# Kernel tuning notes

Hardware: AMD Instinct MI355X
Metric: run time of the kernel (lower is better)

Reference implementation:

```python
import jax, jax.numpy as jnp
import numpy as np

KERNEL = 3
STRIDE = 1
DILATION = 1
EPS = 1e-8


def setup_inputs() -> dict:
    key = jax.random.key(0)
    ks = jax.random.split(key, 7)
    b, dim, dim_out, dim_embed, n = 8, 512, 512, 512, 4
    h = w = 64
    fmap = jax.random.normal(ks[0], (b, dim, h, w), dtype=jnp.float32)
    embed = jax.random.normal(ks[1], (b, dim_embed), dtype=jnp.float32)
    # base conv kernel bank [n, o, i, k, k] (kaiming-normal-ish init)
    fan_in = dim * KERNEL * KERNEL
    weights = jax.random.normal(ks[2], (n, dim_out, dim, KERNEL, KERNEL), dtype=jnp.float32) * np.sqrt(2.0 / fan_in)
    # to_mod: Linear(dim_embed, dim)
    mod_w = jax.random.normal(ks[3], (dim, dim_embed), dtype=jnp.float32) / np.sqrt(dim_embed)
    mod_b = jnp.zeros((dim,), dtype=jnp.float32)
    # to_adaptive_weight: Linear(dim_embed, n)
    adapt_w = jax.random.normal(ks[4], (n, dim_embed), dtype=jnp.float32) / np.sqrt(dim_embed)
    adapt_b = jnp.zeros((n,), dtype=jnp.float32)
    return {"fmap": fmap, "embed": embed, "weights": weights,
            "mod_w": mod_w, "mod_b": mod_b, "adapt_w": adapt_w, "adapt_b": adapt_b}


def reference(fmap, embed, weights, mod_w, mod_b, adapt_w, adapt_b):
    b, _, h, w_sp = fmap.shape
    # adaptive kernel selection: softmax over n kernels, per sample
    sel = jax.nn.softmax(embed @ adapt_w.T + adapt_b, axis=-1)          # [b, n]
    wts = jnp.einsum('noikl,bn->boikl', weights, sel)                   # [b, o, i, k, k]
    # modulation
    mod = embed @ mod_w.T + mod_b                                       # [b, i]
    wts = wts * (mod[:, None, :, None, None] + 1.0)
    # demodulation: normalize each (b, o) filter
    inv_norm = jax.lax.rsqrt(jnp.clip(jnp.sum(wts * wts, axis=(2, 3, 4), keepdims=True), EPS))
    wts = wts * inv_norm
    # grouped conv with groups = b
    pad = ((h - 1) * (STRIDE - 1) + DILATION * (KERNEL - 1)) // 2
    x = fmap.reshape(1, b * fmap.shape[1], h, w_sp)                     # [1, b*i, h, w]
    wg = wts.reshape(b * wts.shape[1], wts.shape[2], KERNEL, KERNEL)    # [b*o, i, k, k]
    out = jax.lax.conv_general_dilated(
        x, wg,
        window_strides=(STRIDE, STRIDE),
        padding=[(pad, pad), (pad, pad)],
        rhs_dilation=(DILATION, DILATION),
        dimension_numbers=('NCHW', 'OIHW', 'NCHW'),
        feature_group_count=b,
    )                                                                   # [1, b*o, h', w']
    return out.reshape(b, -1, out.shape[2], out.shape[3])
```

## Files before the change

kernel.cpp:

```cpp
#include <hip/hip_runtime.h>
#include <stdint.h>

typedef short s16x8 __attribute__((ext_vector_type(8)));
typedef __bf16 bf16x8 __attribute__((ext_vector_type(8)));
typedef float f32x4 __attribute__((ext_vector_type(4)));

#define NB 8
#define DIM 512
#define DIMO 512
#define DEMB 512
#define NKER 4
#define HH 64
#define WW 64
#define HP 66
#define WP 72
#define KTOT 4608
#define NIT 36

__device__ __forceinline__ unsigned short f2bf(float f) {
  unsigned int u = __builtin_bit_cast(unsigned int, f);
  u += 0x7fffu + ((u >> 16) & 1u);
  return (unsigned short)(u >> 16);
}

__global__ void prep_all(const float* __restrict__ fmap,
                         const float* __restrict__ embed,
                         const float* __restrict__ mod_w,
                         const float* __restrict__ mod_b,
                         const float* __restrict__ adapt_w,
                         const float* __restrict__ adapt_b,
                         unsigned short* __restrict__ xt,
                         float* __restrict__ mod, float* __restrict__ sel) {
  const int bid = blockIdx.x;
  const int t = threadIdx.x;

  if (bid < 528) {
    const int b = bid / 66;
    const int yp = bid - b * 66;
    unsigned short* rowb = xt + (((size_t)(b * HP + yp)) * WP) * DIM;
    uint4 z; z.x = 0; z.y = 0; z.z = 0; z.w = 0;

    if (yp == 0 || yp == HP - 1) {
      uint4* p = (uint4*)rowb;
#pragma unroll
      for (int r = 0; r < 18; ++r) p[t + r * 256] = z;
      return;
    }
#pragma unroll
    for (int r = 0; r < 2; ++r) {
      int idx = t + r * 256;
      int pxi = idx >> 6;
      int px = pxi ? (64 + pxi) : 0;
      ((uint4*)(rowb + (size_t)px * DIM))[idx & 63] = z;
    }
    const int x = t & 63;
    const int ic0 = (t >> 6) * 8;
    const float* fb = fmap + (size_t)b * DIM * (HH * WW) + (size_t)(yp - 1) * WW + x;
    unsigned short* ob = rowb + (size_t)(x + 1) * DIM;
    for (int r = 0; r < 16; ++r) {
      int i0 = ic0 + r * 32;
      s16x8 vv;
#pragma unroll
      for (int j = 0; j < 8; ++j)
        vv[j] = (short)f2bf(fb[(size_t)(i0 + j) * (HH * WW)]);
      *(s16x8*)&ob[i0] = vv;
    }
    return;
  }

  const int e9 = bid - 528;
  const int b = e9 / 9;
  const int xc = e9 - b * 9;
  const int lane = t & 63, wv = t >> 6;
  const float* e = embed + (size_t)b * DEMB;

  if (xc == 8) {
    if (wv == 0) {
      float lg[NKER];
#pragma unroll
      for (int n = 0; n < NKER; ++n) {
        const float* ar = adapt_w + (size_t)n * DEMB;
        float s = 0.f;
#pragma unroll
        for (int k = 0; k < 8; ++k) s += e[lane + 64 * k] * ar[lane + 64 * k];
#pragma unroll
        for (int off = 32; off; off >>= 1) s += __shfl_xor(s, off);
        lg[n] = s + adapt_b[n];
      }
      if (lane == 0) {
        float m = lg[0];
#pragma unroll
        for (int n = 1; n < NKER; ++n) m = fmaxf(m, lg[n]);
        float ex[NKER], sum = 0.f;
#pragma unroll
        for (int n = 0; n < NKER; ++n) { ex[n] = expf(lg[n] - m); sum += ex[n]; }
#pragma unroll
        for (int n = 0; n < NKER; ++n) sel[b * NKER + n] = ex[n] / sum;
      }
    }
    return;
  }

  float ev[8];
#pragma unroll
  for (int k = 0; k < 8; ++k) ev[k] = e[lane + 64 * k];
  const int i0 = xc * 64 + wv * 16;
  for (int r = 0; r < 16; ++r) {
    const float* wr = mod_w + (size_t)(i0 + r) * DEMB;
    float s = 0.f;
#pragma unroll
    for (int k = 0; k < 8; ++k) s += ev[k] * wr[lane + 64 * k];
#pragma unroll
    for (int off = 32; off; off >>= 1) s += __shfl_xor(s, off);
    if (lane == 0) mod[b * DIM + i0 + r] = s + mod_b[i0 + r];
  }
}

__global__ void prep_weights(const float* __restrict__ wbank,
                             const float* __restrict__ sel,
                             const float* __restrict__ mod,
                             unsigned short* __restrict__ wts) {
  const int o = blockIdx.x;
  const int t = threadIdx.x;
  extern __shared__ float ls[];
  __shared__ float red[8];

#pragma unroll
  for (int n = 0; n < NKER; ++n) {
    const float* wb = wbank + ((size_t)n * DIMO + o) * (DIM * 9);
#pragma unroll
    for (int r = 0; r < 18; ++r) {
      int ii = t + r * 256;
      ls[n * KTOT + ii] = wb[ii];
    }
  }
  __syncthreads();

  const int lane = t & 63, wv = t >> 6;
  for (int b = 0; b < NB; ++b) {
    const float s0 = sel[b * NKER + 0], s1 = sel[b * NKER + 1];
    const float s2 = sel[b * NKER + 2], s3 = sel[b * NKER + 3];
    const float* mo = mod + b * DIM;
    const int par = (b & 1) << 2;

    float v[18];
    float ss = 0.f;
#pragma unroll
    for (int r = 0; r < 18; ++r) {
      int ok = t + r * 256;
      int src = (ok & 511) * 9 + (ok >> 9);
      float w = s0 * ls[src] + s1 * ls[KTOT + src]
              + s2 * ls[2 * KTOT + src] + s3 * ls[3 * KTOT + src];
      w *= (mo[ok & 511] + 1.0f);
      v[r] = w;
      ss += w * w;
    }
    for (int off = 32; off > 0; off >>= 1) ss += __shfl_down(ss, off);
    if (lane == 0) red[wv + par] = ss;
    __syncthreads();
    float tot = red[0 + par] + red[1 + par] + red[2 + par] + red[3 + par];
    float inv = rsqrtf(fmaxf(tot, 1e-8f));
    unsigned short* wo = wts + ((size_t)(b * DIMO + o)) * KTOT;
#pragma unroll
    for (int r = 0; r < 18; ++r)
      wo[t + r * 256] = f2bf(v[r] * inv);
  }
}

__global__ __launch_bounds__(512, 2) void conv_gemm(
    const unsigned short* __restrict__ wts,
    const unsigned short* __restrict__ xt,
    float* __restrict__ out) {
  extern __shared__ __attribute__((aligned(16))) char smem[];

  const int tid = threadIdx.x;
  const int w = tid >> 6, l = tid & 63;
  const int bid0 = blockIdx.x;
  const int bid = ((bid0 & 7) << 5) | (bid0 >> 3);
  const int b = bid >> 5;
  const int mt = (bid >> 4) & 1;
  const int nt = bid & 15;
  const int orow0 = mt << 8;
  const int prow0 = nt << 8;
  const int y0 = nt << 2;
  const int wm = w >> 2, wn = w & 3;
  const int lr = l & 15, lk = l >> 4;

  const unsigned short* a_base = wts + (size_t)(b * 512 + orow0) * KTOT;
  const unsigned short* x_base = xt + (size_t)b * (HP * WP * DIM);

  const int srow = (w << 3) + (l >> 3);
  const int sx8 = (((l & 7) ^ ((l >> 3) & 7)) << 3);
  const int sw0 = ((lk ^ (l & 7)) << 4);
  const int aRow = (((wm << 6) + lr) << 7);
  const int bRow = (((wn << 5) + lr) << 7);

  int pb[2][2];
#pragma unroll
  for (int h = 0; h < 2; ++h)
#pragma unroll
    for (int j = 0; j < 2; ++j) {
      const int pl = (h << 7) + (j << 6) + srow;
      pb[h][j] = (((y0 + (pl >> 6)) * WP + (pl & 63)) << 9);
    }

  f32x4 acc[2][2][4][2] = {};
  s16x8 aF[2][4], bF0[2][2], bF1[2][2];

  auto stageA = [&](int d, int h, int ks) {
#pragma unroll
    for (int j = 0; j < 2; ++j) {
      const unsigned short* gp = a_base + (size_t)((h << 7) + (j << 6) + srow) * KTOT
                               + (ks << 6) + sx8;
      __builtin_amdgcn_global_load_lds(
          (const __attribute__((address_space(1))) void*)gp,
          (__attribute__((address_space(3))) void*)(smem + (d << 16) + (h << 14) + (j << 13) + (w << 10)),
          16, 0, 0);
    }
  };
  auto stageB = [&](int d, int h, int ks) {
    const int t9 = ks >> 3;
    const int ky = (t9 * 11) >> 5;
    const int koff = ky * (WP << 9) + (t9 - 3 * ky) * 512 + ((ks & 7) << 6);
#pragma unroll
    for (int j = 0; j < 2; ++j) {
      const unsigned short* gp = x_base + pb[h][j] + koff + sx8;
      __builtin_amdgcn_global_load_lds(
          (const __attribute__((address_space(1))) void*)gp,
          (__attribute__((address_space(3))) void*)(smem + (d << 16) + 32768 + (h << 14) + (j << 13) + (w << 10)),
          16, 0, 0);
    }
  };

#define VM4 asm volatile("s_waitcnt vmcnt(4)" ::: "memory")
#define VM2 asm volatile("s_waitcnt vmcnt(2)" ::: "memory")
#define VM0 asm volatile("s_waitcnt vmcnt(0)" ::: "memory")
#define FENCE asm volatile("" ::: "memory")
#define BAR do { FENCE; __builtin_amdgcn_s_barrier(); FENCE; } while (0)

#define LOAD_A(d, mq) \
  _Pragma("unroll") for (int s = 0; s < 2; ++s) \
  _Pragma("unroll") for (int mi = 0; mi < 4; ++mi) \
    aF[s][mi] = *(const s16x8*)(smem + ((d) << 16) + ((mq) << 14) + aRow + (mi << 11) + (sw0 ^ (s << 6)));

#define LOAD_B(d, nq, BF) \
  _Pragma("unroll") for (int s = 0; s < 2; ++s) \
  _Pragma("unroll") for (int nj = 0; nj < 2; ++nj) \
    BF[s][nj] = *(const s16x8*)(smem + ((d) << 16) + 32768 + ((nq) << 14) + bRow + (nj << 11) + (sw0 ^ (s << 6)));

#define MFMA_Q(mq, nq, BF) do { \
  __builtin_amdgcn_s_setprio(1); \
  _Pragma("unroll") for (int s = 0; s < 2; ++s) \
  _Pragma("unroll") for (int mi = 0; mi < 4; ++mi) \
  _Pragma("unroll") for (int nj = 0; nj < 2; ++nj) \
    acc[mq][nq][mi][nj] = __builtin_amdgcn_mfma_f32_16x16x32_bf16( \
        __builtin_bit_cast(bf16x8, aF[s][mi]), __builtin_bit_cast(bf16x8, BF[s][nj]), \
        acc[mq][nq][mi][nj], 0, 0, 0); \
  __builtin_amdgcn_s_setprio(0); \
} while (0)

  stageA(0, 0, 0); stageB(0, 0, 0); stageB(0, 1, 0); stageA(0, 1, 0);
  VM4; BAR;

  for (int it = 0; it < NIT - 1; ++it) {
    const int ks1 = 2 * it + 1, ks2 = 2 * it + 2;
    stageA(1, 0, ks1); LOAD_A(0, 0); LOAD_B(0, 0, bF0); VM4; BAR; MFMA_Q(0, 0, bF0);
    stageB(1, 0, ks1); LOAD_B(0, 1, bF1);               VM4; BAR; MFMA_Q(0, 1, bF1);
    stageB(1, 1, ks1); LOAD_A(0, 1);                         BAR; MFMA_Q(1, 1, bF1);
    stageA(1, 1, ks1);                                  VM4; BAR; MFMA_Q(1, 0, bF0);
    stageA(0, 0, ks2); LOAD_A(1, 0); LOAD_B(1, 0, bF0); VM4; BAR; MFMA_Q(0, 0, bF0);
    stageB(0, 0, ks2); LOAD_B(1, 1, bF1);               VM4; BAR; MFMA_Q(0, 1, bF1);
    stageB(0, 1, ks2); LOAD_A(1, 1);                         BAR; MFMA_Q(1, 1, bF1);
    stageA(0, 1, ks2);                                  VM4; BAR; MFMA_Q(1, 0, bF0);
  }
  {
    const int ks1 = 2 * (NIT - 1) + 1;
    stageA(1, 0, ks1); LOAD_A(0, 0); LOAD_B(0, 0, bF0); VM4; BAR; MFMA_Q(0, 0, bF0);
    stageB(1, 0, ks1); LOAD_B(0, 1, bF1);               VM4; BAR; MFMA_Q(0, 1, bF1);
    stageB(1, 1, ks1); LOAD_A(0, 1);                         BAR; MFMA_Q(1, 1, bF1);
    stageA(1, 1, ks1);                                  VM4; BAR; MFMA_Q(1, 0, bF0);
    LOAD_A(1, 0); LOAD_B(1, 0, bF0);                    VM2; BAR; MFMA_Q(0, 0, bF0);
    LOAD_B(1, 1, bF1);                                  VM0; BAR; MFMA_Q(0, 1, bF1);
    LOAD_A(1, 1);                                            BAR; MFMA_Q(1, 1, bF1);
                                                             BAR; MFMA_Q(1, 0, bF0);
  }

#pragma unroll
  for (int mq = 0; mq < 2; ++mq)
#pragma unroll
  for (int nq = 0; nq < 2; ++nq)
#pragma unroll
  for (int mi = 0; mi < 4; ++mi)
#pragma unroll
  for (int nj = 0; nj < 2; ++nj) {
    float* ob = out
      + ((size_t)(b * 512 + orow0 + (mq << 7) + (wm << 6) + (mi << 4) + (lk << 2)) << 12)
      + prow0 + (nq << 7) + (wn << 5) + (nj << 4) + lr;
#pragma unroll
    for (int q = 0; q < 4; ++q)
      ob[(size_t)q << 12] = acc[mq][nq][mi][nj][q];
  }
#undef VM4
#undef VM2
#undef VM0
#undef FENCE
#undef BAR
#undef LOAD_A
#undef LOAD_B
#undef MFMA_Q
}

extern "C" void kernel_launch(void* const* d_in, const int* in_sizes, int n_in,
                              void* d_out, int out_size, void* d_ws, size_t ws_size,
                              hipStream_t stream) {
  const float* fmap    = (const float*)d_in[0];
  const float* embed   = (const float*)d_in[1];
  const float* wbank   = (const float*)d_in[2];
  const float* mod_w   = (const float*)d_in[3];
  const float* mod_b   = (const float*)d_in[4];
  const float* adapt_w = (const float*)d_in[5];
  const float* adapt_b = (const float*)d_in[6];
  float* out = (float*)d_out;

  char* ws = (char*)d_ws;
  float* sel = (float*)ws;
  float* mod = (float*)(ws + 256);
  unsigned short* wts = (unsigned short*)(ws + 256 + 16384);
  unsigned short* xt  = (unsigned short*)(ws + 256 + 16384 + (size_t)NB * DIMO * KTOT * 2);

  prep_all<<<600, 256, 0, stream>>>(fmap, embed, mod_w, mod_b, adapt_w, adapt_b,
                                    xt, mod, sel);

  (void)hipFuncSetAttribute((const void*)prep_weights,
                            hipFuncAttributeMaxDynamicSharedMemorySize, 73728);
  prep_weights<<<512, 256, 73728, stream>>>(wbank, sel, mod, wts);

  (void)hipFuncSetAttribute((const void*)conv_gemm,
                            hipFuncAttributeMaxDynamicSharedMemorySize, 131072);
  conv_gemm<<<dim3(256), dim3(512), 131072, stream>>>(wts, xt, out);
}
```

Before: 163.6 us.

## Split embed prep and co-schedule fmap transpose with weight prep blocks

Moves the small embed projections into their own tiny kernel and merges the fmap pad/transpose work into the weight-prep kernel. Transpose and weight blocks are interleaved across one 1040-block grid so the two bandwidth-bound phases overlap instead of running back to back. The weight prep also caches each thread's 72 bank values in registers and reads mod once per sample, replacing strided shared-memory reads. Risks: higher register pressure, and the transpose blocks launch with 72KB of dynamic shared memory they never use, which can limit occupancy.

```diff
diff --git a/kernel.cpp b/kernel.cpp
--- a/kernel.cpp
+++ b/kernel.cpp
@@ -23,20 +23,74 @@
   return (unsigned short)(u >> 16);
 }
 
-__global__ void prep_all(const float* __restrict__ fmap,
-                         const float* __restrict__ embed,
-                         const float* __restrict__ mod_w,
-                         const float* __restrict__ mod_b,
-                         const float* __restrict__ adapt_w,
-                         const float* __restrict__ adapt_b,
-                         unsigned short* __restrict__ xt,
-                         float* __restrict__ mod, float* __restrict__ sel) {
+__global__ void prep_embed(const float* __restrict__ embed,
+                           const float* __restrict__ mod_w,
+                           const float* __restrict__ mod_b,
+                           const float* __restrict__ adapt_w,
+                           const float* __restrict__ adapt_b,
+                           float* __restrict__ mod, float* __restrict__ sel) {
+  const int bid = blockIdx.x;
+  const int b = bid / 9;
+  const int xc = bid - b * 9;
+  const int t = threadIdx.x;
+  const int lane = t & 63, wv = t >> 6;
+  const float* e = embed + (size_t)b * DEMB;
+
+  if (xc == 8) {
+    if (wv == 0) {
+      float lg[NKER];
+#pragma unroll
+      for (int n = 0; n < NKER; ++n) {
+        const float* ar = adapt_w + (size_t)n * DEMB;
+        float s = 0.f;
+#pragma unroll
+        for (int k = 0; k < 8; ++k) s += e[lane + 64 * k] * ar[lane + 64 * k];
+#pragma unroll
+        for (int off = 32; off; off >>= 1) s += __shfl_xor(s, off);
+        lg[n] = s + adapt_b[n];
+      }
+      if (lane == 0) {
+        float m = lg[0];
+#pragma unroll
+        for (int n = 1; n < NKER; ++n) m = fmaxf(m, lg[n]);
+        float ex[NKER], sum = 0.f;
+#pragma unroll
+        for (int n = 0; n < NKER; ++n) { ex[n] = expf(lg[n] - m); sum += ex[n]; }
+#pragma unroll
+        for (int n = 0; n < NKER; ++n) sel[b * NKER + n] = ex[n] / sum;
+      }
+    }
+    return;
+  }
+
+  float ev[8];
+#pragma unroll
+  for (int k = 0; k < 8; ++k) ev[k] = e[lane + 64 * k];
+  const int i0 = xc * 64 + wv * 16;
+  for (int r = 0; r < 16; ++r) {
+    const float* wr = mod_w + (size_t)(i0 + r) * DEMB;
+    float s = 0.f;
+#pragma unroll
+    for (int k = 0; k < 8; ++k) s += ev[k] * wr[lane + 64 * k];
+#pragma unroll
+    for (int off = 32; off; off >>= 1) s += __shfl_xor(s, off);
+    if (lane == 0) mod[b * DIM + i0 + r] = s + mod_b[i0 + r];
+  }
+}
+
+__global__ void prep_wf(const float* __restrict__ wbank,
+                        const float* __restrict__ sel,
+                        const float* __restrict__ mod,
+                        const float* __restrict__ fmap,
+                        unsigned short* __restrict__ wts,
+                        unsigned short* __restrict__ xt) {
   const int bid = blockIdx.x;
   const int t = threadIdx.x;
 
-  if (bid < 528) {
-    const int b = bid / 66;
-    const int yp = bid - b * 66;
+  if ((bid & 1) && bid < 1024 ? true : bid >= 1024) {
+    const int f = (bid < 1024) ? (bid >> 1) : (bid - 512);
+    const int b = f / 66;
+    const int yp = f - b * 66;
     unsigned short* rowb = xt + (((size_t)(b * HP + yp)) * WP) * DIM;
     uint4 z; z.x = 0; z.y = 0; z.z = 0; z.w = 0;
 
@@ -68,60 +122,7 @@
     return;
   }
 
-  const int e9 = bid - 528;
-  const int b = e9 / 9;
-  const int xc = e9 - b * 9;
-  const int lane = t & 63, wv = t >> 6;
-  const float* e = embed + (size_t)b * DEMB;
-
-  if (xc == 8) {
-    if (wv == 0) {
-      float lg[NKER];
-#pragma unroll
-      for (int n = 0; n < NKER; ++n) {
-        const float* ar = adapt_w + (size_t)n * DEMB;
-        float s = 0.f;
-#pragma unroll
-        for (int k = 0; k < 8; ++k) s += e[lane + 64 * k] * ar[lane + 64 * k];
-#pragma unroll
-        for (int off = 32; off; off >>= 1) s += __shfl_xor(s, off);
-        lg[n] = s + adapt_b[n];
-      }
-      if (lane == 0) {
-        float m = lg[0];
-#pragma unroll
-        for (int n = 1; n < NKER; ++n) m = fmaxf(m, lg[n]);
-        float ex[NKER], sum = 0.f;
-#pragma unroll
-        for (int n = 0; n < NKER; ++n) { ex[n] = expf(lg[n] - m); sum += ex[n]; }
-#pragma unroll
-        for (int n = 0; n < NKER; ++n) sel[b * NKER + n] = ex[n] / sum;
-      }
-    }
-    return;
-  }
-
-  float ev[8];
-#pragma unroll
-  for (int k = 0; k < 8; ++k) ev[k] = e[lane + 64 * k];
-  const int i0 = xc * 64 + wv * 16;
-  for (int r = 0; r < 16; ++r) {
-    const float* wr = mod_w + (size_t)(i0 + r) * DEMB;
-    float s = 0.f;
-#pragma unroll
-    for (int k = 0; k < 8; ++k) s += ev[k] * wr[lane + 64 * k];
-#pragma unroll
-    for (int off = 32; off; off >>= 1) s += __shfl_xor(s, off);
-    if (lane == 0) mod[b * DIM + i0 + r] = s + mod_b[i0 + r];
-  }
-}
-
-__global__ void prep_weights(const float* __restrict__ wbank,
-                             const float* __restrict__ sel,
-                             const float* __restrict__ mod,
-                             unsigned short* __restrict__ wts) {
-  const int o = blockIdx.x;
-  const int t = threadIdx.x;
+  const int o = bid >> 1;
   extern __shared__ float ls[];
   __shared__ float red[8];
 
@@ -135,24 +136,33 @@
     }
   }
   __syncthreads();
+
+  float wreg[NKER][2][9];
+#pragma unroll
+  for (int n = 0; n < NKER; ++n)
+#pragma unroll
+    for (int p = 0; p < 2; ++p)
+#pragma unroll
+      for (int g = 0; g < 9; ++g)
+        wreg[n][p][g] = ls[n * KTOT + (t + p * 256) * 9 + g];
 
   const int lane = t & 63, wv = t >> 6;
   for (int b = 0; b < NB; ++b) {
     const float s0 = sel[b * NKER + 0], s1 = sel[b * NKER + 1];
     const float s2 = sel[b * NKER + 2], s3 = sel[b * NKER + 3];
-    const float* mo = mod + b * DIM;
+    const float m0 = mod[b * DIM + t] + 1.0f;
+    const float m1 = mod[b * DIM + t + 256] + 1.0f;
     const int par = (b & 1) << 2;
 
-    float v[18];
+    float vv[18];
     float ss = 0.f;
 #pragma unroll
     for (int r = 0; r < 18; ++r) {
-      int ok = t + r * 256;
-      int src = (ok & 511) * 9 + (ok >> 9);
-      float w = s0 * ls[src] + s1 * ls[KTOT + src]
-              + s2 * ls[2 * KTOT + src] + s3 * ls[3 * KTOT + src];
-      w *= (mo[ok & 511] + 1.0f);
-      v[r] = w;
+      const int p = r & 1, g = r >> 1;
+      float w = s0 * wreg[0][p][g] + s1 * wreg[1][p][g]
+              + s2 * wreg[2][p][g] + s3 * wreg[3][p][g];
+      w *= (p ? m1 : m0);
+      vv[r] = w;
       ss += w * w;
     }
     for (int off = 32; off > 0; off >>= 1) ss += __shfl_down(ss, off);
@@ -163,7 +173,7 @@
     unsigned short* wo = wts + ((size_t)(b * DIMO + o)) * KTOT;
 #pragma unroll
     for (int r = 0; r < 18; ++r)
-      wo[t + r * 256] = f2bf(v[r] * inv);
+      wo[t + r * 256] = f2bf(vv[r] * inv);
   }
 }
 
@@ -328,12 +338,11 @@
   unsigned short* wts = (unsigned short*)(ws + 256 + 16384);
   unsigned short* xt  = (unsigned short*)(ws + 256 + 16384 + (size_t)NB * DIMO * KTOT * 2);
 
-  prep_all<<<600, 256, 0, stream>>>(fmap, embed, mod_w, mod_b, adapt_w, adapt_b,
-                                    xt, mod, sel);
-
-  (void)hipFuncSetAttribute((const void*)prep_weights,
+  prep_embed<<<72, 256, 0, stream>>>(embed, mod_w, mod_b, adapt_w, adapt_b, mod, sel);
+
+  (void)hipFuncSetAttribute((const void*)prep_wf,
                             hipFuncAttributeMaxDynamicSharedMemorySize, 73728);
-  prep_weights<<<512, 256, 73728, stream>>>(wbank, sel, mod, wts);
+  prep_wf<<<1040, 256, 73728, stream>>>(wbank, sel, mod, fmap, wts, xt);
 
   (void)hipFuncSetAttribute((const void*)conv_gemm,
                             hipFuncAttributeMaxDynamicSharedMemorySize, 131072);
```

Measured after the change: 168.6 us. 1.03x slower.
